# Optimization experiments

Measured on AMD Instinct MI355X. Metric: run time of the kernel, lower is better.

The kernel has to match this reference:

```python
import jax, jax.numpy as jnp
import numpy as np

B, H, W, C_IN, C_OUT = 32, 128, 128, 128, 128
N_MODES = (32, 32)          # modes kept along each spatial axis
DEG, RANK = 2, 64
M_FRONT = (N_MODES[0] + 1) // 2   # 16: low positive-frequency modes on axis 0
M_BACK = N_MODES[0] - M_FRONT     # 16: high (negative-frequency) modes on axis 0
W_MODES = N_MODES[1] // 2 + 1     # 17: rfft half-spectrum modes on last axis


def _as_complex(p):
    # p: (..., 2) float -> complex
    return jax.lax.complex(p[..., 0], p[..., 1])


def setup_inputs() -> dict:
    key = jax.random.key(0)
    kx, k1, k2, k3, k4 = jax.random.split(key, 5)
    X = jax.random.normal(kx, (B, H, W, C_IN), dtype=jnp.float32)
    # torch.rand on cfloat -> uniform[0,1) real and imag parts
    kout0 = jax.random.uniform(k1, (N_MODES[0], 1, C_OUT, DEG, RANK, 2), dtype=jnp.float32)
    kin0  = jax.random.uniform(k2, (N_MODES[0], 1, C_IN,  DEG, RANK, 2), dtype=jnp.float32)
    kout1 = jax.random.uniform(k3, (1, W_MODES, C_OUT, DEG, RANK, 2), dtype=jnp.float32)
    kin1  = jax.random.uniform(k4, (1, W_MODES, C_IN,  DEG, RANK, 2), dtype=jnp.float32)
    return {"X": X, "kout0": kout0, "kin0": kin0, "kout1": kout1, "kin1": kin1}


def reference(X, kout0, kin0, kout1, kin1):
    ko0, ki0 = _as_complex(kout0), _as_complex(kin0)
    ko1, ki1 = _as_complex(kout1), _as_complex(kin1)
    # low-rank summand per spatial axis: (...idr, ...jdr -> ...ijd)
    S0 = jnp.einsum('...idr,...jdr->...ijd', ko0, ki0)   # (32, 1, O, I, D)
    S1 = jnp.einsum('...idr,...jdr->...ijd', ko1, ki1)   # (1, 17, O, I, D)
    # product over axes, sum over degree d: (32, 17, O, I)
    K = jnp.einsum('...ijd,...ijd->...ij', S0, S1)

    Xf = jnp.fft.rfftn(X, axes=(-3, -2), norm='forward')  # (B, H, W//2+1, C_in) complex
    Y = jnp.zeros(Xf.shape[:-1] + (K.shape[-2],), dtype=jnp.complex64)
    # quadrant 1: low modes on axis 0
    Y = Y.at[:, :M_FRONT, :W_MODES].set(
        jnp.einsum('hwij,bhwj->bhwi', K[:M_FRONT, :W_MODES], Xf[:, :M_FRONT, :W_MODES]))
    # quadrant 2: high (negative-frequency) modes on axis 0
    Y = Y.at[:, -M_BACK:, :W_MODES].set(
        jnp.einsum('hwij,bhwj->bhwi', K[-M_BACK:, :W_MODES], Xf[:, -M_BACK:, :W_MODES]))
    return jnp.fft.irfftn(Y, s=(H, W), axes=(-3, -2), norm='forward')
```

## Files before the change

### kernel.cpp

```cpp
#include <hip/hip_runtime.h>
#include <math.h>

#define PI2 6.283185307179586f


__global__ __launch_bounds__(128) void k_S(
    const float2* __restrict__ ko0, const float2* __restrict__ ki0,
    const float2* __restrict__ ko1, const float2* __restrict__ ki1,
    float4* __restrict__ S0, float4* __restrict__ S1) {
  int bid = blockIdx.x;
  int s = bid >> 7;
  int i = bid & 127;
  int j = threadIdx.x;
  const float2* ko; const float2* ki; float4* S; int si;
  if (s < 32) { ko = ko0; ki = ki0; S = S0; si = s; }
  else        { ko = ko1; ki = ki1; S = S1; si = s - 32; }
  __shared__ float2 koS[2][64];
  koS[j >> 6][j & 63] = ko[(si * 128 + i) * 128 + j];
  __syncthreads();
  const float2* kirow = ki + (si * 128 + j) * 128;
  float2 acc[2];
#pragma unroll
  for (int d = 0; d < 2; d++) {
    float2 a2 = make_float2(0.f, 0.f);
    for (int r = 0; r < 64; r++) {
      float2 a = koS[d][r];
      float2 b = kirow[d * 64 + r];
      a2.x += a.x * b.x - a.y * b.y;
      a2.y += a.x * b.y + a.y * b.x;
    }
    acc[d] = a2;
  }
  S[(si * 128 + i) * 128 + j] = make_float4(acc[0].x, acc[0].y, acc[1].x, acc[1].y);
}

__global__ __launch_bounds__(256) void k_F1(
    const float* __restrict__ X, float2* __restrict__ Xw) {
  __shared__ float2 tw[128];
  int t = threadIdx.x;
  if (t < 128) { float s, c; __sincosf(PI2 * t / 128.f, &s, &c); tw[t] = make_float2(c, s); }
  __syncthreads();
  const char* twc = (const char*)tw;
  int c = t & 127, kg = t >> 7;
  int b = blockIdx.x >> 6;
  int y0 = (blockIdx.x & 63) * 2;
  const float* xr0 = X + ((size_t)(b * 128 + y0) * 128) * 128 + c;
  const float* xr1 = xr0 + 16384;
  float2 a0[9], a1[9];
#pragma unroll
  for (int kk = 0; kk < 9; kk++) { a0[kk] = make_float2(0.f, 0.f); a1[kk] = make_float2(0.f, 0.f); }
  int kb8 = kg * 9 * 8;
  for (int x = 0; x < 128; x++) {
    float v0 = xr0[x * 128];
    float v1 = xr1[x * 128];
#pragma unroll
    for (int kk = 0; kk < 9; kk++) {
      int ob = ((kb8 + kk * 8) * x) & 1016;
      float2 w = *(const float2*)(twc + ob);
      a0[kk].x += v0 * w.x; a0[kk].y -= v0 * w.y;
      a1[kk].x += v1 * w.x; a1[kk].y -= v1 * w.y;
    }
  }
  const float sc = 1.f / 16384.f;
  float2* o0 = Xw + ((size_t)(b * 128 + y0) * 17) * 128 + c;
#pragma unroll
  for (int kk = 0; kk < 9; kk++) {
    int k = kg * 9 + kk;
    if (k < 17) {
      o0[k * 128] = make_float2(a0[kk].x * sc, a0[kk].y * sc);
      o0[2176 + k * 128] = make_float2(a1[kk].x * sc, a1[kk].y * sc);
    }
  }
}

__global__ __launch_bounds__(256) void k_F2(
    const float2* __restrict__ Xw, float2* __restrict__ Xf) {
  __shared__ float2 tw[128];
  int t = threadIdx.x;
  if (t < 128) { float s, c; __sincosf(PI2 * t / 128.f, &s, &c); tw[t] = make_float2(c, s); }
  __syncthreads();
  const char* twc = (const char*)tw;
  int b = blockIdx.x / 17, k = blockIdx.x - b * 17;
  int c = t & 127, hh = t >> 7;
  float2 acc[16];
#pragma unroll
  for (int q = 0; q < 16; q++) acc[q] = make_float2(0.f, 0.f);
  int hb8 = hh ? 112 * 8 : 0;
  const float2* xp = Xw + ((size_t)(b * 128) * 17 + k) * 128 + c;
  for (int y = 0; y < 128; y++) {
    float2 xv = xp[(size_t)y * 2176];
#pragma unroll
    for (int q = 0; q < 16; q++) {
      int ob = ((hb8 + q * 8) * y) & 1016;
      float2 w = *(const float2*)(twc + ob);
      acc[q].x += xv.x * w.x + xv.y * w.y;
      acc[q].y += xv.y * w.x - xv.x * w.y;
    }
  }
  float2* op = Xf + ((size_t)(b * 32 + hh * 16) * 17 + k) * 128 + c;
#pragma unroll
  for (int q = 0; q < 16; q++) op[(size_t)q * 2176] = acc[q];
}

__global__ __launch_bounds__(256) void k_spec(
    const float4* __restrict__ S0, const float4* __restrict__ S1,
    const float2* __restrict__ Xf, float2* __restrict__ Y) {
  __shared__ float2 Xs[32][128];
  __shared__ float2 Ks[16][129];
  int m = blockIdx.x;
  int hm = m / 17, w = m - hm * 17;
  int t = threadIdx.x;
  for (int q = t; q < 32 * 128; q += 256) {
    int b = q >> 7, j = q & 127;
    Xs[b][j] = Xf[((size_t)(b * 32 + hm) * 17 + w) * 128 + j];
  }
  const float4* s0p = S0 + (size_t)hm * 16384;
  const float4* s1p = S1 + (size_t)w * 16384;
  int i = t & 127, bh = t >> 7;
  float2 acc[16];
#pragma unroll
  for (int bb = 0; bb < 16; bb++) acc[bb] = make_float2(0.f, 0.f);
  for (int jt = 0; jt < 128; jt += 16) {
    __syncthreads();
    for (int q = t; q < 16 * 128; q += 256) {
      int ii = q >> 4, jj = q & 15;
      float4 a = s0p[ii * 128 + jt + jj];
      float4 b4 = s1p[ii * 128 + jt + jj];
      Ks[jj][ii] = make_float2(a.x * b4.x - a.y * b4.y + a.z * b4.z - a.w * b4.w,
                               a.x * b4.y + a.y * b4.x + a.z * b4.w + a.w * b4.z);
    }
    __syncthreads();
#pragma unroll 4
    for (int jj = 0; jj < 16; jj++) {
      float2 kv = Ks[jj][i];
#pragma unroll
      for (int bb = 0; bb < 16; bb++) {
        float2 xv = Xs[bh * 16 + bb][jt + jj];
        acc[bb].x += kv.x * xv.x - kv.y * xv.y;
        acc[bb].y += kv.x * xv.y + kv.y * xv.x;
      }
    }
  }
#pragma unroll
  for (int bb = 0; bb < 16; bb++) {
    int b = bh * 16 + bb;
    Y[((size_t)(b * 32 + hm) * 17 + w) * 128 + i] = acc[bb];
  }
}

__global__ __launch_bounds__(256) void k_I1(
    const float2* __restrict__ Y, float2* __restrict__ Q) {
  __shared__ float2 tw[128];
  int t = threadIdx.x;
  if (t < 128) { float s, c; __sincosf(PI2 * t / 128.f, &s, &c); tw[t] = make_float2(c, s); }
  __syncthreads();
  const char* twc = (const char*)tw;
  int b = blockIdx.x / 17, k = blockIdx.x - b * 17;
  int o = t & 127, yh = t >> 7;
  float2 v[32];
#pragma unroll
  for (int hm = 0; hm < 32; hm++)
    v[hm] = Y[((size_t)(b * 32 + hm) * 17 + k) * 128 + o];
  float2* qp = Q + ((size_t)(b * 128) * 17 + k) * 128 + o;
  for (int yy = 0; yy < 64; yy++) {
    int y = yh * 64 + yy;
    float2 a = make_float2(0.f, 0.f);
#pragma unroll
    for (int hm = 0; hm < 32; hm++) {
      const int h8 = (hm < 16 ? hm : hm + 96) * 8;
      int ob = (h8 * y) & 1016;
      float2 w = *(const float2*)(twc + ob);
      a.x += v[hm].x * w.x - v[hm].y * w.y;
      a.y += v[hm].x * w.y + v[hm].y * w.x;
    }
    qp[(size_t)y * 2176] = a;
  }
}

__global__ __launch_bounds__(256) void k_I2(
    const float2* __restrict__ Q, float* __restrict__ out) {
  __shared__ float2 tw[128];
  int t = threadIdx.x;
  if (t < 128) { float s, c; __sincosf(PI2 * t / 128.f, &s, &c); tw[t] = make_float2(c, s); }
  __syncthreads();
  const char* twc = (const char*)tw;
  int b = blockIdx.x >> 6;
  int y0 = (blockIdx.x & 63) * 2;
  int o = t & 127, xh = t >> 7;
  const float2* q0p = Q + ((size_t)(b * 128 + y0) * 17) * 128 + o;
  float2 q0[17], q1[17];
#pragma unroll
  for (int k = 0; k < 17; k++) {
    float wgt = (k == 0) ? 1.f : 2.f;
    float2 v0 = q0p[k * 128];
    float2 v1 = q0p[2176 + k * 128];
    q0[k] = make_float2(v0.x * wgt, v0.y * wgt);
    q1[k] = make_float2(v1.x * wgt, v1.y * wgt);
  }
  float* o0 = out + ((size_t)(b * 128 + y0) * 128) * 128 + o;
  float* o1 = o0 + 16384;
  for (int xx = 0; xx < 64; xx++) {
    int x = xh * 64 + xx;
    float s0 = 0.f, s1 = 0.f;
#pragma unroll
    for (int k = 0; k < 17; k++) {
      int ob = (k * 8 * x) & 1016;
      float2 w = *(const float2*)(twc + ob);
      s0 += q0[k].x * w.x - q0[k].y * w.y;
      s1 += q1[k].x * w.x - q1[k].y * w.y;
    }
    o0[x * 128] = s0;
    o1[x * 128] = s1;
  }
}

extern "C" void kernel_launch(void* const* d_in, const int* in_sizes, int n_in,
                              void* d_out, int out_size, void* d_ws, size_t ws_size,
                              hipStream_t stream) {
  (void)in_sizes; (void)n_in; (void)out_size;
  const float*  X     = (const float*)d_in[0];
  const float2* kout0 = (const float2*)d_in[1];
  const float2* kin0  = (const float2*)d_in[2];
  const float2* kout1 = (const float2*)d_in[3];
  const float2* kin1  = (const float2*)d_in[4];
  float* out = (float*)d_out;

  float2* ws = (float2*)d_ws;
  const size_t NA = 8912896;
  float2* A  = ws;
  float2* S0 = ws + NA;
  float2* S1 = S0 + 1048576;
  float2* Xf = S1 + 557056;
  float2* Yk = Xf + 2228224;
  const size_t need = (NA + 1048576 + 557056 + 2 * 2228224) * sizeof(float2);
  if (ws_size < need) return;

  k_S   <<<49 * 128, 128, 0, stream>>>(kout0, kin0, kout1, kin1,
                                       (float4*)S0, (float4*)S1);
  k_F1  <<<32 * 64, 256, 0, stream>>>(X, A);
  k_F2  <<<32 * 17, 256, 0, stream>>>(A, Xf);
  k_spec<<<544, 256, 0, stream>>>((const float4*)S0, (const float4*)S1, Xf, Yk);
  k_I1  <<<32 * 17, 256, 0, stream>>>(Yk, A);
  k_I2  <<<32 * 64, 256, 0, stream>>>(A, out);
}
```

Baseline: 1.048 ms.

## Rebalance DFT kernels: vectorize F1 channels, split F2/I1 grids for more blocks

k_F1 now has each thread handle two adjacent channels with float2 loads and float4 stores. Its frequency bins are interleaved across four thread groups, which removes the wasted 18th bin slot of the old 9+9 split. k_F2 and k_I1 launch twice as many blocks (1088 instead of 544), each doing half the output modes or rows, so more of the GPU's compute units are kept busy. The cost is redundant input loads in k_F2 and k_I1, plus uneven work in k_F1, where group 0 computes 5 bins and the other groups compute 4.

```diff
diff --git a/kernel.cpp b/kernel.cpp
--- a/kernel.cpp
+++ b/kernel.cpp
@@ -41,34 +41,45 @@
   if (t < 128) { float s, c; __sincosf(PI2 * t / 128.f, &s, &c); tw[t] = make_float2(c, s); }
   __syncthreads();
   const char* twc = (const char*)tw;
-  int c = t & 127, kg = t >> 7;
+  int cp = t & 63, kg = t >> 6;
   int b = blockIdx.x >> 6;
   int y0 = (blockIdx.x & 63) * 2;
-  const float* xr0 = X + ((size_t)(b * 128 + y0) * 128) * 128 + c;
-  const float* xr1 = xr0 + 16384;
-  float2 a0[9], a1[9];
-#pragma unroll
-  for (int kk = 0; kk < 9; kk++) { a0[kk] = make_float2(0.f, 0.f); a1[kk] = make_float2(0.f, 0.f); }
-  int kb8 = kg * 9 * 8;
+  const float2* x0 = (const float2*)X + ((size_t)(b * 128 + y0) * 128) * 64 + cp;
+  float2 a[2][5][2];
+#pragma unroll
+  for (int r = 0; r < 2; r++)
+#pragma unroll
+    for (int kk = 0; kk < 5; kk++) {
+      a[r][kk][0] = make_float2(0.f, 0.f);
+      a[r][kk][1] = make_float2(0.f, 0.f);
+    }
   for (int x = 0; x < 128; x++) {
-    float v0 = xr0[x * 128];
-    float v1 = xr1[x * 128];
-#pragma unroll
-    for (int kk = 0; kk < 9; kk++) {
-      int ob = ((kb8 + kk * 8) * x) & 1016;
-      float2 w = *(const float2*)(twc + ob);
-      a0[kk].x += v0 * w.x; a0[kk].y -= v0 * w.y;
-      a1[kk].x += v1 * w.x; a1[kk].y -= v1 * w.y;
+    float2 v0 = x0[x * 64];
+    float2 v1 = x0[8192 + x * 64];
+#pragma unroll
+    for (int kk = 0; kk < 5; kk++) {
+      if (kk < 4 || kg == 0) {
+        int k8 = (kg + 4 * kk) * 8;
+        int ob = (k8 * x) & 1016;
+        float2 w = *(const float2*)(twc + ob);
+        a[0][kk][0].x += v0.x * w.x; a[0][kk][0].y -= v0.x * w.y;
+        a[0][kk][1].x += v0.y * w.x; a[0][kk][1].y -= v0.y * w.y;
+        a[1][kk][0].x += v1.x * w.x; a[1][kk][0].y -= v1.x * w.y;
+        a[1][kk][1].x += v1.y * w.x; a[1][kk][1].y -= v1.y * w.y;
+      }
     }
   }
   const float sc = 1.f / 16384.f;
-  float2* o0 = Xw + ((size_t)(b * 128 + y0) * 17) * 128 + c;
-#pragma unroll
-  for (int kk = 0; kk < 9; kk++) {
-    int k = kg * 9 + kk;
-    if (k < 17) {
-      o0[k * 128] = make_float2(a0[kk].x * sc, a0[kk].y * sc);
-      o0[2176 + k * 128] = make_float2(a1[kk].x * sc, a1[kk].y * sc);
+#pragma unroll
+  for (int r = 0; r < 2; r++) {
+#pragma unroll
+    for (int kk = 0; kk < 5; kk++) {
+      if (kk < 4 || kg == 0) {
+        int k = kg + 4 * kk;
+        float4* dst = (float4*)(Xw + ((size_t)((b * 128 + y0 + r) * 17 + k)) * 128 + 2 * cp);
+        *dst = make_float4(a[r][kk][0].x * sc, a[r][kk][0].y * sc,
+                           a[r][kk][1].x * sc, a[r][kk][1].y * sc);
+      }
     }
   }
 }
@@ -80,26 +91,33 @@
   if (t < 128) { float s, c; __sincosf(PI2 * t / 128.f, &s, &c); tw[t] = make_float2(c, s); }
   __syncthreads();
   const char* twc = (const char*)tw;
-  int b = blockIdx.x / 17, k = blockIdx.x - b * 17;
+  int bk = blockIdx.x >> 1, mh = blockIdx.x & 1;
+  int b = bk / 17, k = bk - b * 17;
   int c = t & 127, hh = t >> 7;
-  float2 acc[16];
-#pragma unroll
-  for (int q = 0; q < 16; q++) acc[q] = make_float2(0.f, 0.f);
-  int hb8 = hh ? 112 * 8 : 0;
+  int g = mh * 2 + hh;
+  int h8[8];
+#pragma unroll
+  for (int q = 0; q < 8; q++) {
+    int hm = g * 8 + q;
+    h8[q] = (hm < 16 ? hm : hm + 96) * 8;
+  }
+  float2 acc[8];
+#pragma unroll
+  for (int q = 0; q < 8; q++) acc[q] = make_float2(0.f, 0.f);
   const float2* xp = Xw + ((size_t)(b * 128) * 17 + k) * 128 + c;
   for (int y = 0; y < 128; y++) {
     float2 xv = xp[(size_t)y * 2176];
 #pragma unroll
-    for (int q = 0; q < 16; q++) {
-      int ob = ((hb8 + q * 8) * y) & 1016;
+    for (int q = 0; q < 8; q++) {
+      int ob = (h8[q] * y) & 1016;
       float2 w = *(const float2*)(twc + ob);
       acc[q].x += xv.x * w.x + xv.y * w.y;
       acc[q].y += xv.y * w.x - xv.x * w.y;
     }
   }
-  float2* op = Xf + ((size_t)(b * 32 + hh * 16) * 17 + k) * 128 + c;
-#pragma unroll
-  for (int q = 0; q < 16; q++) op[(size_t)q * 2176] = acc[q];
+  float2* op = Xf + ((size_t)(b * 32 + g * 8) * 17 + k) * 128 + c;
+#pragma unroll
+  for (int q = 0; q < 8; q++) op[(size_t)q * 2176] = acc[q];
 }
 
 __global__ __launch_bounds__(256) void k_spec(
@@ -155,15 +173,17 @@
   if (t < 128) { float s, c; __sincosf(PI2 * t / 128.f, &s, &c); tw[t] = make_float2(c, s); }
   __syncthreads();
   const char* twc = (const char*)tw;
-  int b = blockIdx.x / 17, k = blockIdx.x - b * 17;
+  int bk = blockIdx.x >> 1, yq = blockIdx.x & 1;
+  int b = bk / 17, k = bk - b * 17;
   int o = t & 127, yh = t >> 7;
+  int ybase = yq * 64 + yh * 32;
   float2 v[32];
 #pragma unroll
   for (int hm = 0; hm < 32; hm++)
     v[hm] = Y[((size_t)(b * 32 + hm) * 17 + k) * 128 + o];
   float2* qp = Q + ((size_t)(b * 128) * 17 + k) * 128 + o;
-  for (int yy = 0; yy < 64; yy++) {
-    int y = yh * 64 + yy;
+  for (int yy = 0; yy < 32; yy++) {
+    int y = ybase + yy;
     float2 a = make_float2(0.f, 0.f);
 #pragma unroll
     for (int hm = 0; hm < 32; hm++) {
@@ -238,8 +258,8 @@
   k_S   <<<49 * 128, 128, 0, stream>>>(kout0, kin0, kout1, kin1,
                                        (float4*)S0, (float4*)S1);
   k_F1  <<<32 * 64, 256, 0, stream>>>(X, A);
-  k_F2  <<<32 * 17, 256, 0, stream>>>(A, Xf);
+  k_F2  <<<32 * 17 * 2, 256, 0, stream>>>(A, Xf);
   k_spec<<<544, 256, 0, stream>>>((const float4*)S0, (const float4*)S1, Xf, Yk);
-  k_I1  <<<32 * 17, 256, 0, stream>>>(Yk, A);
+  k_I1  <<<32 * 17 * 2, 256, 0, stream>>>(Yk, A);
   k_I2  <<<32 * 64, 256, 0, stream>>>(A, out);
 }
```

Result: faster. 1.018 ms (-2.9%).
